# Performance work log

Hardware: AMD Instinct MI355X
Metric: run time of the kernel (lower is better)

## Reference

```python
import jax, jax.numpy as jnp
import numpy as np

EPS = 1e-5

def conv2d(x, w, stride=1, padding=0, bias=None):
    out = jax.lax.conv_general_dilated(
        x, w, (stride, stride), [(padding, padding), (padding, padding)],
        dimension_numbers=('NCHW', 'OIHW', 'NCHW'))
    if bias is not None:
        out = out + bias[None, :, None, None]
    return out

def bn_relu(x, gamma, beta, mean, var):
    scale = gamma / jnp.sqrt(var + EPS)
    return jax.nn.relu(x * scale[None, :, None, None]
                       + (beta - mean * scale)[None, :, None, None])

def deform_conv(x, wp, bp, wc, ks, pad, stride):
    # Canonical DeformConv2d (v1, modulation=False) from pytorch-deform-conv-v2.
    b, c, H, W = x.shape
    N = ks * ks
    offset = conv2d(x, wp, stride=stride, padding=1, bias=bp)        # (b,2N,h,w)
    h, w = offset.shape[2], offset.shape[3]
    xp = jnp.pad(x, ((0, 0), (0, 0), (pad, pad), (pad, pad)))        # zero_padding
    Hp, Wp = H + 2 * pad, W + 2 * pad
    off = offset.transpose(0, 2, 3, 1)                               # (b,h,w,2N)
    rng = jnp.arange(-(ks - 1) // 2, (ks - 1) // 2 + 1, dtype=x.dtype)
    pnx, pny = jnp.meshgrid(rng, rng, indexing='ij')
    pnx, pny = pnx.reshape(-1), pny.reshape(-1)                      # (N,)
    p0x = jnp.arange(1, h * stride + 1, stride, dtype=x.dtype)       # torch starts at 1
    p0y = jnp.arange(1, w * stride + 1, stride, dtype=x.dtype)
    px = p0x[None, :, None, None] + pnx[None, None, None, :] + off[..., :N]  # (b,h,w,N)
    py = p0y[None, None, :, None] + pny[None, None, None, :] + off[..., N:]
    qx0 = jnp.floor(jax.lax.stop_gradient(px))
    qy0 = jnp.floor(jax.lax.stop_gradient(py))
    qx0c = jnp.clip(qx0, 0, Hp - 1).astype(jnp.int32)
    qx1c = jnp.clip(qx0 + 1, 0, Hp - 1).astype(jnp.int32)
    qy0c = jnp.clip(qy0, 0, Wp - 1).astype(jnp.int32)
    qy1c = jnp.clip(qy0 + 1, 0, Wp - 1).astype(jnp.int32)
    pxc = jnp.clip(px, 0, Hp - 1)
    pyc = jnp.clip(py, 0, Wp - 1)
    fx0 = qx0c.astype(x.dtype); fx1 = qx1c.astype(x.dtype)
    fy0 = qy0c.astype(x.dtype); fy1 = qy1c.astype(x.dtype)
    g_lt = (1 + (fx0 - pxc)) * (1 + (fy0 - pyc))
    g_rb = (1 - (fx1 - pxc)) * (1 - (fy1 - pyc))
    g_lb = (1 + (fx0 - pxc)) * (1 - (fy1 - pyc))
    g_rt = (1 - (fx1 - pxc)) * (1 + (fy0 - pyc))
    xf = xp.reshape(b, c, Hp * Wp)
    def gather(qx, qy):
        idx = (qx * Wp + qy).reshape(b, 1, h * w * N)
        return jnp.take_along_axis(xf, idx, axis=2).reshape(b, c, h, w, N)
    x_off = (g_lt[:, None] * gather(qx0c, qy0c)
             + g_rb[:, None] * gather(qx1c, qy1c)
             + g_lb[:, None] * gather(qx0c, qy1c)
             + g_rt[:, None] * gather(qx1c, qy0c))                   # (b,c,h,w,N)
    # stride=ks conv over the reshaped (h*ks, w*ks) map == einsum over sample slot n
    return jnp.einsum('bchwn,ocn->bohw', x_off, wc.reshape(wc.shape[0], c, N))

def setup_inputs() -> dict:
    key = jax.random.key(0)
    ks = iter(jax.random.split(key, 40))
    def nrm(shape, scale):
        return jax.random.normal(next(ks), shape, dtype=jnp.float32) * scale
    def he(shape):  # fan_in = prod of all but first dim
        return nrm(shape, float(np.sqrt(2.0 / np.prod(shape[1:]))))
    def bn(c):
        return (jnp.ones((c,), jnp.float32) + nrm((c,), 0.05),  # gamma
                nrm((c,), 0.05),                                 # beta
                nrm((c,), 0.1),                                  # running mean
                jax.random.uniform(next(ks), (c,), jnp.float32, 0.5, 1.5))  # var
    inp = {'x': jax.random.normal(next(ks), (256, 3, 32, 32), dtype=jnp.float32)}
    inp['w1'] = he((32, 3, 3, 3)); inp['b1'] = nrm((32,), 0.01)
    inp['g1'], inp['be1'], inp['m1'], inp['v1'] = bn(32)
    inp['wp2'] = nrm((18, 32, 3, 3), 0.01); inp['bp2'] = nrm((18,), 0.001)
    inp['wc2'] = he((64, 32, 3, 3))
    inp['g2'], inp['be2'], inp['m2'], inp['v2'] = bn(64)
    inp['wp3'] = nrm((18, 64, 3, 3), 0.01); inp['bp3'] = nrm((18,), 0.001)
    inp['wc3'] = he((128, 64, 3, 3))
    inp['g3'], inp['be3'], inp['m3'], inp['v3'] = bn(128)
    inp['wp4'] = nrm((18, 128, 3, 3), 0.01); inp['bp4'] = nrm((18,), 0.001)
    inp['wc4'] = he((128, 128, 3, 3))
    inp['g4'], inp['be4'], inp['m4'], inp['v4'] = bn(128)
    inp['wcls'] = nrm((100, 128), float(1.0 / np.sqrt(128)))
    inp['bcls'] = nrm((100,), 0.01)
    return inp

def reference(x, w1, b1, g1, be1, m1, v1,
              wp2, bp2, wc2, g2, be2, m2, v2,
              wp3, bp3, wc3, g3, be3, m3, v3,
              wp4, bp4, wc4, g4, be4, m4, v4,
              wcls, bcls):
    h = bn_relu(conv2d(x, w1, stride=1, padding=1, bias=b1), g1, be1, m1, v1)   # (b,32,32,32)
    h = bn_relu(deform_conv(h, wp2, bp2, wc2, 3, 1, 2), g2, be2, m2, v2)        # (b,64,16,16)
    h = bn_relu(deform_conv(h, wp3, bp3, wc3, 3, 1, 1), g3, be3, m3, v3)        # (b,128,16,16)
    h = bn_relu(deform_conv(h, wp4, bp4, wc4, 3, 1, 2), g4, be4, m4, v4)        # (b,128,8,8)
    h = jnp.mean(h, axis=(2, 3))                                                # avg_pool2d(8) -> (b,128)
    return h @ wcls.T + bcls[None, :]
```

## Files before the change

### kernel.cpp

```cpp
#include <hip/hip_runtime.h>
#include <math.h>

#define BN_EPS 1e-5f

typedef __attribute__((ext_vector_type(4))) float f4;
typedef __attribute__((ext_vector_type(4))) int i4v;
typedef __attribute__((ext_vector_type(8))) short short8;
typedef __attribute__((ext_vector_type(4))) float f32x4;
typedef _Float16 half4v __attribute__((ext_vector_type(4)));

__device__ inline unsigned short f2bf(float f) {
    unsigned int u = __builtin_bit_cast(unsigned int, f);
    return (unsigned short)((u + 0x7FFFu + ((u >> 16) & 1u)) >> 16);
}
__device__ inline float blo(int u) { return __builtin_bit_cast(float, (int)(u << 16)); }
__device__ inline float bhi(int u) { return __builtin_bit_cast(float, (int)(u & 0xffff0000)); }
__device__ inline int pkbf_fast(float hi, float lo) {
    unsigned uh = __builtin_bit_cast(unsigned, hi) + 0x8000u;
    unsigned ul = __builtin_bit_cast(unsigned, lo) + 0x8000u;
    return (int)__builtin_amdgcn_perm(uh, ul, 0x07060302u);
}

struct CvtSeg { const float* src; unsigned short* dst; int oreal, c, kpad, end; };
struct CvtArgs { CvtSeg s[7]; };

__global__ __launch_bounds__(256)
void cvt_all(CvtArgs a)
{
    int idx = blockIdx.x * 256 + threadIdx.x;
    int base = 0;
    #pragma unroll
    for (int i = 0; i < 7; ++i) {
        if (idx < a.s[i].end) {
            int local = idx - base;
            int kpad = a.s[i].kpad, c = a.s[i].c;
            int o = local / kpad, k = local - o * kpad;
            unsigned short val = 0;
            if (o < a.s[i].oreal && k < 9 * c) {
                int n = k / c, cc = k - n * c;
                val = f2bf(a.s[i].src[(o * c + cc) * 9 + n]);
            }
            a.s[i].dst[local] = val;
            return;
        }
        base = a.s[i].end;
    }
}

__global__ __launch_bounds__(256)
void conv1_tile(const float* __restrict__ x, const unsigned short* __restrict__ wq,
                const float* __restrict__ bias, const float* __restrict__ g,
                const float* __restrict__ be, const float* __restrict__ m,
                const float* __restrict__ v, unsigned short* __restrict__ out)
{
    __shared__ __align__(16) float img[3072];
    __shared__ __align__(16) unsigned short wt[32 * 40];
    __shared__ float scb[32], shb[32];
    const int tid = threadIdx.x;
    const int b = blockIdx.x >> 2;
    const int qtr = blockIdx.x & 3;
    if (tid < 32) {
        float sc = g[tid] * rsqrtf(v[tid] + BN_EPS);
        scb[tid] = sc;
        shb[tid] = be[tid] - m[tid] * sc + bias[tid] * sc;
    }
    *(ushort4*)&wt[(tid >> 3) * 40 + (tid & 7) * 4] =
        *(const ushort4*)(wq + (tid >> 3) * 32 + (tid & 7) * 4);
    const float* xb = x + (size_t)b * 3072;
    #pragma unroll
    for (int r = 0; r < 3; ++r) {
        int idx = r * 256 + tid;
        *(f4*)&img[idx * 4] = *(const f4*)(xb + idx * 4);
    }
    __syncthreads();
    const int wid = tid >> 6, lane = tid & 63, quad = lane >> 4, m16 = lane & 15;
    short8 af0 = *(const short8*)&wt[m16 * 40 + quad * 8];
    short8 af1 = *(const short8*)&wt[(16 + m16) * 40 + quad * 8];
    #pragma unroll
    for (int it = 0; it < 4; ++it) {
        int pix = qtr * 256 + it * 64 + wid * 16 + m16;
        int i = pix >> 5, j = pix & 31;
        short8 bfrag;
        #pragma unroll
        for (int jj = 0; jj < 8; ++jj) {
            int k = quad * 8 + jj;
            float val = 0.f;
            if (k < 27) {
                int n = k / 3, c = k - n * 3;
                int u = i - 1 + n / 3, vv = j - 1 + n % 3;
                if (u >= 0 && u < 32 && vv >= 0 && vv < 32)
                    val = img[c * 1024 + u * 32 + vv];
            }
            bfrag[jj] = (short)f2bf(val);
        }
        f32x4 a0 = {0.f,0.f,0.f,0.f}, a1 = {0.f,0.f,0.f,0.f};
        a0 = __builtin_amdgcn_mfma_f32_16x16x32_bf16(af0, bfrag, a0, 0, 0, 0);
        a1 = __builtin_amdgcn_mfma_f32_16x16x32_bf16(af1, bfrag, a1, 0, 0, 0);
        unsigned short* op = out + ((size_t)b * 1024 + pix) * 32;
        ushort4 s0, s1;
        #pragma unroll
        for (int rr = 0; rr < 4; ++rr) {
            int o0 = quad * 4 + rr, o1 = 16 + quad * 4 + rr;
            ((unsigned short*)&s0)[rr] = f2bf(fmaxf(fmaf(a0[rr], scb[o0], shb[o0]), 0.f));
            ((unsigned short*)&s1)[rr] = f2bf(fmaxf(fmaf(a1[rr], scb[o1], shb[o1]), 0.f));
        }
        *(ushort4*)(op + quad * 4) = s0;
        *(ushort4*)(op + 16 + quad * 4) = s1;
    }
}

template<int C, int OREAL, int OPAD, int H, int W, int OH, int OW, int S,
         int MTILE, int OBLK>
__global__ __launch_bounds__(256, 4)
void dconv_fused(const unsigned short* __restrict__ xact,
                 const unsigned short* __restrict__ wp, const float* __restrict__ bp,
                 const unsigned short* __restrict__ wc,
                 const float* __restrict__ g, const float* __restrict__ be,
                 const float* __restrict__ m, const float* __restrict__ v,
                 unsigned short* __restrict__ out)
{
    constexpr int K = C * 9;
    constexpr int KCH = C / 32;
    constexpr int OPB = OPAD / OBLK;
    constexpr int OT = OPB / 64;
    constexpr int ST = MTILE / 16;
    constexpr int PWP = (MTILE >= 32) ? MTILE / 2 : MTILE;
    constexpr int STP = PWP / 16;
    constexpr int CP = C + 8;
    constexpr int GL = C / 8;
    constexpr int NGRP = 256 / GL;
    constexpr int NT = MTILE / NGRP;
    constexpr int OHW = OH * OW;
    constexpr int HWC = H * W * C;
    constexpr int Hp = H + 2, Wpp = W + 2;
    static_assert(MTILE % NGRP == 0 && OPB % 64 == 0 && STP >= 1, "tiling");

    __shared__ __align__(16) unsigned short xo[2][MTILE * CP];
    __shared__ __align__(8) ushort4   tab_p[MTILE][9];
    __shared__ __align__(8) _Float16  tab_h[MTILE][9][4];
    __shared__ _Float16 off_lds[MTILE][20];
    __shared__ int imgb[MTILE];
    __shared__ float scb[OPAD], shb[OPAD];

    const int tid = threadIdx.x;
    const int ob  = blockIdx.x % OBLK;
    const int p0  = (blockIdx.x / OBLK) * MTILE;

    if (tid < MTILE) imgb[tid] = ((p0 + tid) / OHW) * HWC;
    for (int o = tid; o < OREAL; o += 256) {
        float sc = g[o] * rsqrtf(v[o] + BN_EPS);
        scb[o] = sc;
        shb[o] = be[o] - m[o] * sc;
    }
    for (int e = tid; e < MTILE * 9; e += 256) {
        int lp = e / 9, n = e % 9;
        int p = p0 + lp;
        int rem = p % OHW;
        int i = rem / OW, j = rem % OW;
        int u = i * S - 1 + n / 3, vv = j * S - 1 + n % 3;
        bool ok = (u >= 0 && u < H && vv >= 0 && vv < W);
        ushort4 tp;
        tp.x = ok ? (unsigned short)((u * W + vv) * C) : (unsigned short)0;
        tp.y = ok ? (unsigned short)0xFFFF : (unsigned short)0;
        tp.z = 0; tp.w = 0;
        tab_p[lp][n] = tp;
    }
    __syncthreads();

    const int gl = tid % GL, grp = tid / GL;
    const int wid = tid >> 6, lane = tid & 63, quad = lane >> 4, m16 = lane & 15;

    {
        const int ogp = wid & 1;
        const int pgp = (MTILE >= 32) ? (wid >> 1) : 0;
        const int obp = ogp * 16;
        const int pbp = pgp * PWP;
        i4v Tp[NT];
        auto issueA = [&](int n) {
            #pragma unroll
            for (int it = 0; it < NT; ++it) {
                const int pix = it * NGRP + grp;
                Tp[it] = *(const i4v*)(xact + imgb[pix] + gl * 8 + (int)tab_p[pix][n].x);
            }
        };
        auto commitA = [&](int n, int buf) {
            #pragma unroll
            for (int it = 0; it < NT; ++it) {
                const int pix = it * NGRP + grp;
                int mask = (int)(short)tab_p[pix][n].y;
                i4v R;
                #pragma unroll
                for (int e2 = 0; e2 < 4; ++e2) R[e2] = Tp[it][e2] & mask;
                *(i4v*)&xo[buf][pix * CP + gl * 8] = R;
            }
        };
        auto loadWp = [&](int n, short8* wf) {
            #pragma unroll
            for (int ch = 0; ch < KCH; ++ch)
                wf[ch] = *(const short8*)(wp + (size_t)(obp + m16) * K
                                          + n * C + ch * 32 + quad * 8);
        };
        f32x4 accp[STP];
        #pragma unroll
        for (int st = 0; st < STP; ++st) accp[st] = (f32x4){0.f, 0.f, 0.f, 0.f};
        short8 wfA[KCH], wfB[KCH];
        issueA(0);
        loadWp(0, wfA);
        commitA(0, 0);
        __syncthreads();
        for (int n = 0; n < 9; ++n) {
            const int cur = n & 1;
            if (n < 8) { issueA(n + 1); loadWp(n + 1, wfB); }
            #pragma unroll
            for (int ch = 0; ch < KCH; ++ch)
                #pragma unroll
                for (int st = 0; st < STP; ++st) {
                    short8 bf = *(const short8*)&xo[cur][(pbp + st * 16 + m16) * CP
                                                        + ch * 32 + quad * 8];
                    accp[st] = __builtin_amdgcn_mfma_f32_16x16x32_bf16(
                        wfA[ch], bf, accp[st], 0, 0, 0);
                }
            if (n < 8) {
                commitA(n + 1, cur ^ 1);
                #pragma unroll
                for (int ch = 0; ch < KCH; ++ch) wfA[ch] = wfB[ch];
            }
            __syncthreads();
        }
        #pragma unroll
        for (int st = 0; st < STP; ++st) {
            int pix = pbp + st * 16 + m16;
            #pragma unroll
            for (int rr = 0; rr < 4; ++rr) {
                int o = obp + quad * 4 + rr;
                if (o < 18) off_lds[pix][o] = (_Float16)(accp[st][rr] + bp[o]);
            }
        }
    }
    __syncthreads();

    for (int e = tid; e < MTILE * 9; e += 256) {
        int lp = e / 9, n = e % 9;
        int p = p0 + lp;
        int rem = p % OHW;
        int i = rem / OW, j = rem % OW;
        float ox = (float)off_lds[lp][n];
        float oy = (float)off_lds[lp][9 + n];
        float px = (float)(i * S + n / 3) + ox;
        float py = (float)(j * S + n % 3) + oy;
        int qx0 = (int)floorf(px), qy0 = (int)floorf(py);
        int x0 = min(max(qx0, 0), Hp - 1), x1 = min(max(qx0 + 1, 0), Hp - 1);
        int y0 = min(max(qy0, 0), Wpp - 1), y1 = min(max(qy0 + 1, 0), Wpp - 1);
        float pxc = fminf(fmaxf(px, 0.f), (float)(Hp - 1));
        float pyc = fminf(fmaxf(py, 0.f), (float)(Wpp - 1));
        float gx0 = 1.f + ((float)x0 - pxc), gx1 = 1.f - ((float)x1 - pxc);
        float gy0 = 1.f + ((float)y0 - pyc), gy1 = 1.f - ((float)y1 - pyc);
        int u0 = x0 - 1, u1 = x1 - 1, v0 = y0 - 1, v1 = y1 - 1;
        bool k0 = (u0 >= 0 && u0 < H && v0 >= 0 && v0 < W);
        bool k1 = (u1 >= 0 && u1 < H && v1 >= 0 && v1 < W);
        bool k2 = (u0 >= 0 && u0 < H && v1 >= 0 && v1 < W);
        bool k3 = (u1 >= 0 && u1 < H && v0 >= 0 && v0 < W);
        ushort4 tp;
        tp.x = k0 ? (unsigned short)((u0 * W + v0) * C) : (unsigned short)0;
        tp.y = k1 ? (unsigned short)((u1 * W + v1) * C) : (unsigned short)0;
        tp.z = k2 ? (unsigned short)((u0 * W + v1) * C) : (unsigned short)0;
        tp.w = k3 ? (unsigned short)((u1 * W + v0) * C) : (unsigned short)0;
        tab_p[lp][n] = tp;
        half4v hw;
        hw[0] = (_Float16)(k0 ? gx0 * gy0 : 0.f);
        hw[1] = (_Float16)(k1 ? gx1 * gy1 : 0.f);
        hw[2] = (_Float16)(k2 ? gx0 * gy1 : 0.f);
        hw[3] = (_Float16)(k3 ? gx1 * gy0 : 0.f);
        *(half4v*)&tab_h[lp][n][0] = hw;
    }
    __syncthreads();

    {
        const int obase = ob * OPB + wid * OT * 16;
        i4v T[NT][4];
        auto issueC = [&](int n) {
            #pragma unroll
            for (int it = 0; it < NT; ++it) {
                const int pix = it * NGRP + grp;
                const unsigned short* xb = xact + imgb[pix] + gl * 8;
                ushort4 tp = tab_p[pix][n];
                T[it][0] = *(const i4v*)(xb + tp.x);
                T[it][1] = *(const i4v*)(xb + tp.y);
                T[it][2] = *(const i4v*)(xb + tp.z);
                T[it][3] = *(const i4v*)(xb + tp.w);
            }
        };
        auto commitC = [&](int n, int buf) {
            #pragma unroll
            for (int it = 0; it < NT; ++it) {
                const int pix = it * NGRP + grp;
                half4v hw = *(const half4v*)&tab_h[pix][n][0];
                float w0 = (float)hw[0], w1 = (float)hw[1];
                float w2 = (float)hw[2], w3 = (float)hw[3];
                i4v R;
                #pragma unroll
                for (int e2 = 0; e2 < 4; ++e2) {
                    float lo = w0 * blo(T[it][0][e2]);
                    lo = fmaf(w1, blo(T[it][1][e2]), lo);
                    lo = fmaf(w2, blo(T[it][2][e2]), lo);
                    lo = fmaf(w3, blo(T[it][3][e2]), lo);
                    float hi = w0 * bhi(T[it][0][e2]);
                    hi = fmaf(w1, bhi(T[it][1][e2]), hi);
                    hi = fmaf(w2, bhi(T[it][2][e2]), hi);
                    hi = fmaf(w3, bhi(T[it][3][e2]), hi);
                    R[e2] = pkbf_fast(hi, lo);
                }
                *(i4v*)&xo[buf][pix * CP + gl * 8] = R;
            }
        };
        auto loadWc = [&](int n, short8 (*wf)[OT]) {
            #pragma unroll
            for (int ch = 0; ch < KCH; ++ch)
                #pragma unroll
                for (int t = 0; t < OT; ++t)
                    wf[ch][t] = *(const short8*)(wc + (size_t)(obase + t * 16 + m16) * K
                                                 + n * C + ch * 32 + quad * 8);
        };

        f32x4 acc[ST][OT];
        #pragma unroll
        for (int st = 0; st < ST; ++st)
            #pragma unroll
            for (int t = 0; t < OT; ++t) acc[st][t] = (f32x4){0.f, 0.f, 0.f, 0.f};

        short8 wfA[KCH][OT], wfB[KCH][OT];
        issueC(0);
        loadWc(0, wfA);
        commitC(0, 0);
        __syncthreads();

        for (int n = 0; n < 9; ++n) {
            const int cur = n & 1;
            if (n < 8) {
                issueC(n + 1);
                loadWc(n + 1, wfB);
            }
            #pragma unroll
            for (int ch = 0; ch < KCH; ++ch)
                #pragma unroll
                for (int st = 0; st < ST; ++st) {
                    short8 bf = *(const short8*)&xo[cur][(st * 16 + m16) * CP
                                                        + ch * 32 + quad * 8];
                    #pragma unroll
                    for (int t = 0; t < OT; ++t)
                        acc[st][t] = __builtin_amdgcn_mfma_f32_16x16x32_bf16(
                            wfA[ch][t], bf, acc[st][t], 0, 0, 0);
                }
            if (n < 8) {
                commitC(n + 1, cur ^ 1);
                #pragma unroll
                for (int ch = 0; ch < KCH; ++ch)
                    #pragma unroll
                    for (int t = 0; t < OT; ++t) wfA[ch][t] = wfB[ch][t];
            }
            __syncthreads();
        }

        #pragma unroll
        for (int st = 0; st < ST; ++st) {
            const int p = p0 + st * 16 + m16;
            #pragma unroll
            for (int t = 0; t < OT; ++t) {
                int o = obase + t * 16 + quad * 4;
                ushort4 s;
                #pragma unroll
                for (int rr = 0; rr < 4; ++rr)
                    ((unsigned short*)&s)[rr] =
                        f2bf(fmaxf(fmaf(acc[st][t][rr], scb[o + rr], shb[o + rr]), 0.f));
                *(ushort4*)(out + (size_t)p * OPAD + o) = s;
            }
        }
    }
}

__global__ __launch_bounds__(128)
void pool_fc(const unsigned short* __restrict__ h4, const float* __restrict__ wcls,
             const float* __restrict__ bcls, float* __restrict__ out)
{
    __shared__ float pool[128];
    int b = blockIdx.x;
    int tid = threadIdx.x;
    const unsigned short* src = h4 + (size_t)b * 8192;
    float s = 0.f;
    #pragma unroll
    for (int t = 0; t < 64; ++t)
        s += __builtin_bit_cast(float, (unsigned)src[t * 128 + tid] << 16);
    pool[tid] = s * (1.f / 64.f);
    __syncthreads();
    if (tid < 100) {
        float acc = bcls[tid];
        const float* wr = wcls + tid * 128;
        #pragma unroll
        for (int c = 0; c < 128; ++c) acc = fmaf(pool[c], wr[c], acc);
        out[(size_t)b * 100 + tid] = acc;
    }
}

extern "C" void kernel_launch(void* const* d_in, const int* in_sizes, int n_in,
                              void* d_out, int out_size, void* d_ws, size_t ws_size,
                              hipStream_t stream)
{
    const float* x    = (const float*)d_in[0];
    const float* w1   = (const float*)d_in[1];
    const float* b1   = (const float*)d_in[2];
    const float* g1   = (const float*)d_in[3];
    const float* be1  = (const float*)d_in[4];
    const float* m1   = (const float*)d_in[5];
    const float* v1   = (const float*)d_in[6];
    const float* wp2  = (const float*)d_in[7];
    const float* bp2  = (const float*)d_in[8];
    const float* wc2  = (const float*)d_in[9];
    const float* g2   = (const float*)d_in[10];
    const float* be2  = (const float*)d_in[11];
    const float* m2   = (const float*)d_in[12];
    const float* v2   = (const float*)d_in[13];
    const float* wp3  = (const float*)d_in[14];
    const float* bp3  = (const float*)d_in[15];
    const float* wc3  = (const float*)d_in[16];
    const float* g3   = (const float*)d_in[17];
    const float* be3  = (const float*)d_in[18];
    const float* m3   = (const float*)d_in[19];
    const float* v3   = (const float*)d_in[20];
    const float* wp4  = (const float*)d_in[21];
    const float* bp4  = (const float*)d_in[22];
    const float* wc4  = (const float*)d_in[23];
    const float* g4   = (const float*)d_in[24];
    const float* be4  = (const float*)d_in[25];
    const float* m4   = (const float*)d_in[26];
    const float* v4   = (const float*)d_in[27];
    const float* wcls = (const float*)d_in[28];
    const float* bcls = (const float*)d_in[29];
    float* out = (float*)d_out;

    unsigned short* h1 = (unsigned short*)d_ws;
    unsigned short* h2 = h1 + 8388608;
    unsigned short* h3 = h2 + 4194304;
    unsigned short* h4 = h3 + 8388608;
    unsigned short* wc2b = h4 + 2097152;
    unsigned short* wc3b = wc2b + 18432;
    unsigned short* wc4b = wc3b + 73728;
    unsigned short* wp2b = wc4b + 147456;
    unsigned short* wp3b = wp2b + 9216;
    unsigned short* wp4b = wp3b + 18432;
    unsigned short* wq1  = wp4b + 36864;
    (void)ws_size; (void)in_sizes; (void)n_in; (void)out_size;

    CvtArgs ca;
    ca.s[0] = { wc2, wc2b, 64, 32, 288, 18432 };
    ca.s[1] = { wc3, wc3b, 128, 64, 576, 92160 };
    ca.s[2] = { wc4, wc4b, 128, 128, 1152, 239616 };
    ca.s[3] = { wp2, wp2b, 18, 32, 288, 248832 };
    ca.s[4] = { wp3, wp3b, 18, 64, 576, 267264 };
    ca.s[5] = { wp4, wp4b, 18, 128, 1152, 304128 };
    ca.s[6] = { w1, wq1, 32, 3, 32, 305152 };
    cvt_all<<<1192, 256, 0, stream>>>(ca);

    conv1_tile<<<1024, 256, 0, stream>>>(x, wq1, b1, g1, be1, m1, v1, h1);

    dconv_fused<32, 64, 64, 32, 32, 16, 16, 2, 64, 1><<<1024, 256, 0, stream>>>(
        h1, wp2b, bp2, wc2b, g2, be2, m2, v2, h2);

    dconv_fused<64, 128, 128, 16, 16, 16, 16, 1, 64, 1><<<1024, 256, 0, stream>>>(
        h2, wp3b, bp3, wc3b, g3, be3, m3, v3, h3);

    dconv_fused<128, 128, 128, 16, 16, 8, 8, 2, 32, 2><<<1024, 256, 0, stream>>>(
        h3, wp4b, bp4, wc4b, g4, be4, m4, v4, h4);

    pool_fc<<<256, 128, 0, stream>>>(h4, wcls, bcls, out);
}
```

Measured before the change: 243.7 us.

## Stage whole input image in LDS for last deformable conv layer

Adds a dconv_img kernel for the third deformable conv. Each block copies one image's full 16x16x128 bf16 activation map (64KB) into shared memory, computes the offsets with MFMA, then does the bilinear gathers from LDS and runs the main conv MFMA over half the output channels. The grid drops to 512 blocks (two per image). The aim is to replace scattered global gathers with LDS reads, at the cost of large LDS use per block, which may limit occupancy, and of computing the offset conv twice per image.

```diff
diff --git a/kernel.cpp b/kernel.cpp
--- a/kernel.cpp
+++ b/kernel.cpp
@@ -374,6 +374,175 @@
                         f2bf(fmaxf(fmaf(acc[st][t][rr], scb[o + rr], shb[o + rr]), 0.f));
                 *(ushort4*)(out + (size_t)p * OPAD + o) = s;
             }
+        }
+    }
+}
+
+template<int C, int O, int H, int W, int OH, int OW, int S>
+__global__ __launch_bounds__(256, 2)
+void dconv_img(const unsigned short* __restrict__ xact,
+               const unsigned short* __restrict__ wp, const float* __restrict__ bp,
+               const unsigned short* __restrict__ wc,
+               const float* __restrict__ g, const float* __restrict__ be,
+               const float* __restrict__ m, const float* __restrict__ v,
+               unsigned short* __restrict__ out)
+{
+    constexpr int K = C * 9;
+    constexpr int KCH = C / 32;
+    constexpr int NPIX = OH * OW;
+    constexpr int ST = NPIX / 16;
+    constexpr int HWC = H * W * C;
+    constexpr int Hp = H + 2, Wpp = W + 2;
+
+    __shared__ __align__(16) unsigned short img[HWC];
+    __shared__ _Float16 off_lds[NPIX][20];
+    __shared__ float scb[O], shb[O];
+
+    const int tid = threadIdx.x;
+    const int b  = blockIdx.x >> 1;
+    const int ob = blockIdx.x & 1;
+
+    const unsigned short* srcim = xact + (size_t)b * HWC;
+    #pragma unroll
+    for (int it = 0; it < HWC / 2048; ++it) {
+        int idx = (it * 256 + tid) * 8;
+        *(i4v*)&img[idx] = *(const i4v*)(srcim + idx);
+    }
+    for (int o = tid; o < O; o += 256) {
+        float sc = g[o] * rsqrtf(v[o] + BN_EPS);
+        scb[o] = sc;
+        shb[o] = be[o] - m[o] * sc;
+    }
+    __syncthreads();
+
+    const int wid = tid >> 6, lane = tid & 63, quad = lane >> 4, m16 = lane & 15;
+
+    {
+        const int pl = wid * 16 + m16;
+        const int i = pl / OW, j = pl % OW;
+        f32x4 accp[2] = {{0.f,0.f,0.f,0.f},{0.f,0.f,0.f,0.f}};
+        short8 wfA[KCH][2], wfB[KCH][2];
+        auto loadWp = [&](int n, short8 (*wf)[2]) {
+            #pragma unroll
+            for (int ch = 0; ch < KCH; ++ch)
+                #pragma unroll
+                for (int t = 0; t < 2; ++t)
+                    wf[ch][t] = *(const short8*)(wp + (size_t)(t * 16 + m16) * K
+                                                 + n * C + ch * 32 + quad * 8);
+        };
+        loadWp(0, wfA);
+        for (int n = 0; n < 9; ++n) {
+            if (n < 8) loadWp(n + 1, wfB);
+            int u = i * S - 1 + n / 3, vv = j * S - 1 + n % 3;
+            bool ok = (u >= 0 && u < H && vv >= 0 && vv < W);
+            int ta = ok ? (u * W + vv) * C : 0;
+            int mask = ok ? -1 : 0;
+            #pragma unroll
+            for (int ch = 0; ch < KCH; ++ch) {
+                i4v A = *(const i4v*)&img[ta + ch * 32 + quad * 8];
+                i4v R;
+                #pragma unroll
+                for (int e2 = 0; e2 < 4; ++e2) R[e2] = A[e2] & mask;
+                short8 bf = __builtin_bit_cast(short8, R);
+                accp[0] = __builtin_amdgcn_mfma_f32_16x16x32_bf16(wfA[ch][0], bf, accp[0], 0, 0, 0);
+                accp[1] = __builtin_amdgcn_mfma_f32_16x16x32_bf16(wfA[ch][1], bf, accp[1], 0, 0, 0);
+            }
+            if (n < 8) {
+                #pragma unroll
+                for (int ch = 0; ch < KCH; ++ch) {
+                    wfA[ch][0] = wfB[ch][0];
+                    wfA[ch][1] = wfB[ch][1];
+                }
+            }
+        }
+        #pragma unroll
+        for (int t = 0; t < 2; ++t)
+            #pragma unroll
+            for (int rr = 0; rr < 4; ++rr) {
+                int o = t * 16 + quad * 4 + rr;
+                if (o < 18) off_lds[pl][o] = (_Float16)(accp[t][rr] + bp[o]);
+            }
+    }
+    __syncthreads();
+
+    {
+        const int obase = ob * (O / 2) + wid * 16;
+        f32x4 acc[ST];
+        #pragma unroll
+        for (int st = 0; st < ST; ++st) acc[st] = (f32x4){0.f, 0.f, 0.f, 0.f};
+        short8 wfA[KCH], wfB[KCH];
+        auto loadWc = [&](int n, short8* wf) {
+            #pragma unroll
+            for (int ch = 0; ch < KCH; ++ch)
+                wf[ch] = *(const short8*)(wc + (size_t)(obase + m16) * K
+                                          + n * C + ch * 32 + quad * 8);
+        };
+        loadWc(0, wfA);
+        for (int n = 0; n < 9; ++n) {
+            if (n < 8) loadWc(n + 1, wfB);
+            #pragma unroll
+            for (int st = 0; st < ST; ++st) {
+                const int pl = st * 16 + m16;
+                const int i = pl / OW, j = pl % OW;
+                float ox = (float)off_lds[pl][n];
+                float oy = (float)off_lds[pl][9 + n];
+                float px = (float)(i * S + n / 3) + ox;
+                float py = (float)(j * S + n % 3) + oy;
+                int qx0 = (int)floorf(px), qy0 = (int)floorf(py);
+                int x0 = min(max(qx0, 0), Hp - 1), x1 = min(max(qx0 + 1, 0), Hp - 1);
+                int y0 = min(max(qy0, 0), Wpp - 1), y1 = min(max(qy0 + 1, 0), Wpp - 1);
+                float pxc = fminf(fmaxf(px, 0.f), (float)(Hp - 1));
+                float pyc = fminf(fmaxf(py, 0.f), (float)(Wpp - 1));
+                float gx0 = 1.f + ((float)x0 - pxc), gx1 = 1.f - ((float)x1 - pxc);
+                float gy0 = 1.f + ((float)y0 - pyc), gy1 = 1.f - ((float)y1 - pyc);
+                int u0 = x0 - 1, u1 = x1 - 1, v0 = y0 - 1, v1 = y1 - 1;
+                bool k0 = (u0 >= 0 && u0 < H && v0 >= 0 && v0 < W);
+                bool k1 = (u1 >= 0 && u1 < H && v1 >= 0 && v1 < W);
+                bool k2 = (u0 >= 0 && u0 < H && v1 >= 0 && v1 < W);
+                bool k3 = (u1 >= 0 && u1 < H && v0 >= 0 && v0 < W);
+                int t0 = k0 ? (u0 * W + v0) * C : 0;  float w0 = k0 ? gx0 * gy0 : 0.f;
+                int t1 = k1 ? (u1 * W + v1) * C : 0;  float w1 = k1 ? gx1 * gy1 : 0.f;
+                int t2 = k2 ? (u0 * W + v1) * C : 0;  float w2 = k2 ? gx0 * gy1 : 0.f;
+                int t3 = k3 ? (u1 * W + v0) * C : 0;  float w3 = k3 ? gx1 * gy0 : 0.f;
+                #pragma unroll
+                for (int ch = 0; ch < KCH; ++ch) {
+                    const int cb = ch * 32 + quad * 8;
+                    i4v A  = *(const i4v*)&img[t0 + cb];
+                    i4v Bv = *(const i4v*)&img[t1 + cb];
+                    i4v Cv = *(const i4v*)&img[t2 + cb];
+                    i4v Dv = *(const i4v*)&img[t3 + cb];
+                    i4v R;
+                    #pragma unroll
+                    for (int e2 = 0; e2 < 4; ++e2) {
+                        float lo = w0 * blo(A[e2]);
+                        lo = fmaf(w1, blo(Bv[e2]), lo);
+                        lo = fmaf(w2, blo(Cv[e2]), lo);
+                        lo = fmaf(w3, blo(Dv[e2]), lo);
+                        float hi = w0 * bhi(A[e2]);
+                        hi = fmaf(w1, bhi(Bv[e2]), hi);
+                        hi = fmaf(w2, bhi(Cv[e2]), hi);
+                        hi = fmaf(w3, bhi(Dv[e2]), hi);
+                        R[e2] = pkbf_fast(hi, lo);
+                    }
+                    short8 bf = __builtin_bit_cast(short8, R);
+                    acc[st] = __builtin_amdgcn_mfma_f32_16x16x32_bf16(wfA[ch], bf, acc[st], 0, 0, 0);
+                }
+            }
+            if (n < 8) {
+                #pragma unroll
+                for (int ch = 0; ch < KCH; ++ch) wfA[ch] = wfB[ch];
+            }
+        }
+        #pragma unroll
+        for (int st = 0; st < ST; ++st) {
+            const int pl = st * 16 + m16;
+            int o = obase + quad * 4;
+            ushort4 s;
+            #pragma unroll
+            for (int rr = 0; rr < 4; ++rr)
+                ((unsigned short*)&s)[rr] =
+                    f2bf(fmaxf(fmaf(acc[st][rr], scb[o + rr], shb[o + rr]), 0.f));
+            *(ushort4*)(out + ((size_t)b * NPIX + pl) * O + o) = s;
         }
     }
 }
@@ -468,7 +637,7 @@
     dconv_fused<64, 128, 128, 16, 16, 16, 16, 1, 64, 1><<<1024, 256, 0, stream>>>(
         h2, wp3b, bp3, wc3b, g3, be3, m3, v3, h3);
 
-    dconv_fused<128, 128, 128, 16, 16, 8, 8, 2, 32, 2><<<1024, 256, 0, stream>>>(
+    dconv_img<128, 128, 16, 16, 8, 8, 2><<<512, 256, 0, stream>>>(
         h3, wp4b, bp4, wc4b, g4, be4, m4, v4, h4);
 
     pool_fc<<<256, 128, 0, stream>>>(h4, wcls, bcls, out);
```

Result: slower. 282.0 us (+15.7%).
